# Optimization experiments

Hardware: AMD Instinct MI355X
Metric: run time of the kernel (lower is better)

Reference implementation:

```python
import jax, jax.numpy as jnp
import numpy as np

# Static multi-scale feature pyramid shapes (value_shapes arg of MSDeformAttn.forward)
VALUE_SHAPES = ((80, 80), (40, 40), (20, 20), (10, 10))
N_HEADS, N_LEVELS, N_POINTS, D_MODEL = 8, 4, 4, 256


def setup_inputs() -> dict:
    key = jax.random.key(0)
    ks = jax.random.split(key, 11)
    bs, lq, d = 16, 1000, D_MODEL
    lv = sum(h * w for h, w in VALUE_SHAPES)  # 8500
    s = 0.02  # weight scale
    f32 = jnp.float32
    return {
        "query": jax.random.normal(ks[0], (bs, lq, d), f32),
        "refer_bbox": jax.random.uniform(ks[1], (bs, lq, 1, 4), f32),  # cxcywh in [0,1]
        "value": jax.random.normal(ks[2], (bs, lv, d), f32),
        "W_off": jax.random.normal(ks[3], (d, N_HEADS * N_LEVELS * N_POINTS * 2), f32) * s,
        "b_off": jax.random.normal(ks[4], (N_HEADS * N_LEVELS * N_POINTS * 2,), f32) * s,
        "W_attn": jax.random.normal(ks[5], (d, N_HEADS * N_LEVELS * N_POINTS), f32) * s,
        "b_attn": jax.random.normal(ks[6], (N_HEADS * N_LEVELS * N_POINTS,), f32) * s,
        "W_val": jax.random.normal(ks[7], (d, d), f32) * s,
        "b_val": jax.random.normal(ks[8], (d,), f32) * s,
        "W_out": jax.random.normal(ks[9], (d, d), f32) * s,
        "b_out": jax.random.normal(ks[10], (d,), f32) * s,
    }


def _bilinear_sample(v, x, y):
    """grid_sample(mode=bilinear, padding=zeros, align_corners=False) equivalent.
    v: [bs, H, W, nh, dh]; x, y: pixel-space coords [bs, lq, nh, P].
    Returns [bs, lq, nh, P, dh]."""
    bs, H, W, nh, dh = v.shape
    x0f = jnp.floor(x)
    y0f = jnp.floor(y)
    wx = x - x0f  # fractional weights
    wy = y - y0f
    x0 = x0f.astype(jnp.int32)
    y0 = y0f.astype(jnp.int32)
    x1, y1 = x0 + 1, y0 + 1
    b_idx = jnp.arange(bs)[:, None, None, None]
    h_idx = jnp.arange(nh)[None, None, :, None]

    def gather(yi, xi):
        valid = (xi >= 0) & (xi < W) & (yi >= 0) & (yi < H)
        xc = jnp.clip(xi, 0, W - 1)
        yc = jnp.clip(yi, 0, H - 1)
        val = v[b_idx, yc, xc, h_idx]  # [bs, lq, nh, P, dh]
        return val * valid[..., None].astype(v.dtype)

    return (gather(y0, x0) * ((1 - wx) * (1 - wy))[..., None]
            + gather(y0, x1) * (wx * (1 - wy))[..., None]
            + gather(y1, x0) * ((1 - wx) * wy)[..., None]
            + gather(y1, x1) * (wx * wy)[..., None])


def reference(query, refer_bbox, value, W_off, b_off, W_attn, b_attn, W_val, b_val, W_out, b_out):
    bs, lq, d = query.shape
    nh, L, P = N_HEADS, N_LEVELS, N_POINTS
    dh = d // nh

    # value projection
    v = value @ W_val + b_val  # [bs, lv, d]
    v = v.reshape(bs, -1, nh, dh)

    # sampling offsets and attention weights from query
    offsets = (query @ W_off + b_off).reshape(bs, lq, nh, L, P, 2)
    attn = (query @ W_attn + b_attn).reshape(bs, lq, nh, L * P)
    attn = jax.nn.softmax(attn, axis=-1).reshape(bs, lq, nh, L, P)

    # refer_bbox: [bs, lq, 1, 4] cxcywh; num_points == 4 branch
    add = offsets / P * refer_bbox[:, :, None, :, None, 2:] * 0.5
    loc = refer_bbox[:, :, None, :, None, :2] + add  # [bs, lq, nh, L, P, 2] in [0,1]

    out = jnp.zeros((bs, lq, nh, dh), query.dtype)
    start = 0
    for l, (H, W) in enumerate(VALUE_SHAPES):
        vl = v[:, start:start + H * W].reshape(bs, H, W, nh, dh)
        start += H * W
        ll = loc[:, :, :, l]  # [bs, lq, nh, P, 2]
        # normalized [0,1] -> pixel coords (align_corners=False): p = loc*size - 0.5
        x = ll[..., 0] * W - 0.5
        y = ll[..., 1] * H - 0.5
        sampled = _bilinear_sample(vl, x, y)  # [bs, lq, nh, P, dh]
        out = out + jnp.einsum('bqhpd,bqhp->bqhd', sampled, attn[:, :, :, l])

    out = out.reshape(bs, lq, d)
    return out @ W_out + b_out
```

## Files before the change

### kernel.cpp

```cpp
#include <hip/hip_runtime.h>
#include <cstdint>
#include <cstddef>


typedef unsigned short u16;
typedef u16 u16x8 __attribute__((ext_vector_type(8)));
typedef __bf16 bf16x8 __attribute__((ext_vector_type(8)));
typedef float f32x4 __attribute__((ext_vector_type(4)));

__device__ inline u16 f2bf(float f) {
  return __builtin_bit_cast(u16, (__bf16)f);
}

__device__ __forceinline__ void glds16(const void* g, void* l) {
  __builtin_amdgcn_global_load_lds(
      (const __attribute__((address_space(1))) void*)g,
      (__attribute__((address_space(3))) void*)l, 16, 0, 0);
}

__global__ __launch_bounds__(256) void wconv(
    const float* __restrict__ W0, const float* __restrict__ W1,
    const float* __restrict__ W2, const float* __restrict__ W3,
    u16* __restrict__ T0, u16* __restrict__ T1, u16* __restrict__ T2,
    u16* __restrict__ T3) {
  __shared__ u16 tile[64][65];
  const float* Ws[4] = {W0, W1, W2, W3};
  u16* Ts[4] = {T0, T1, T2, T3};
  const int Ns[4] = {256, 256, 128, 256};
  const int z = blockIdx.z;
  const int N = Ns[z];
  const int n0 = blockIdx.x * 64;
  if (n0 >= N) return;
  const int k0 = blockIdx.y * 64;
  const float* W = Ws[z];
  u16* Wt = Ts[z];
  const int tr = threadIdx.x >> 6;
  const int tc = threadIdx.x & 63;
#pragma unroll
  for (int r = 0; r < 64; r += 4)
    tile[r + tr][tc] = f2bf(W[(size_t)(k0 + r + tr) * N + n0 + tc]);
  __syncthreads();
#pragma unroll
  for (int r = 0; r < 64; r += 4)
    Wt[(size_t)(n0 + r + tr) * 256 + k0 + tc] = tile[tc][r + tr];
}

template <int NF, bool OUT_BF16>
__global__ __launch_bounds__(256, 1) void gemm_pers(
    const float* __restrict__ A, const u16* __restrict__ Wt,
    const float* __restrict__ bias, void* __restrict__ Cv,
    int M, int NT, int G) {
  constexpr int N = NF * 16;
  __shared__ __align__(16) u16 Bls[N * 256];
  __shared__ __align__(16) float Asub[4 * 2 * 1024];
  const int wave = threadIdx.x >> 6;
  const int lane = threadIdx.x & 63;
  const int lr = lane & 15;
  const int lj = lane >> 4;

#pragma unroll
  for (int g = 0; g < NF * 2; ++g) {
    int inst = wave * NF * 2 + g;
    int s = inst * 2 + (lane >> 5);
    int pc = lane & 31;
    int jc = pc ^ (s & 7);
    int c = (s & 15) * NF + (s >> 4);
    glds16((const char*)Wt + (size_t)c * 512 + (size_t)jc * 16,
           (char*)Bls + inst * 1024);
  }

  float bv[NF];
#pragma unroll
  for (int ni = 0; ni < NF; ++ni) bv[ni] = bias[lr * NF + ni];

  char* aw = (char*)Asub + wave * 8192;

  auto stageA = [&](int t, int s, int buf) {
#pragma unroll
    for (int i = 0; i < 4; ++i) {
      long row = (long)t * 128 + wave * 32 + i * 8 + (lane >> 3);
      if (row > (long)M - 1) row = M - 1;
      int jc = (lane & 7) ^ (lane >> 3);
      glds16((const char*)A + row * 1024 + (size_t)s * 128 + (size_t)jc * 16,
             aw + buf * 4096 + i * 1024);
    }
  };

  stageA(blockIdx.x, 0, 0);
  stageA(blockIdx.x, 1, 1);
  __syncthreads();

  for (int t = blockIdx.x; t < NT; t += G) {
    f32x4 acc[2][NF] = {};
#pragma unroll
    for (int s = 0; s < 8; ++s) {
      if (s == 0 || s == 1)
        asm volatile("s_waitcnt vmcnt(20)" ::: "memory");
      else if (s == 2)
        asm volatile("s_waitcnt vmcnt(8)" ::: "memory");
      else
        asm volatile("s_waitcnt vmcnt(4)" ::: "memory");
      const char* ab = aw + (s & 1) * 4096;
      bf16x8 af[2];
#pragma unroll
      for (int rg = 0; rg < 2; ++rg) {
        int row = rg * 16 + lr;
        int sw = lane & 7;
        int j0 = lj * 2;
        f32x4 a0 = *(const f32x4*)(ab + row * 128 + ((j0 ^ sw) * 16));
        f32x4 a1 = *(const f32x4*)(ab + row * 128 + (((j0 + 1) ^ sw) * 16));
        bf16x8 v;
        v[0] = (__bf16)a0[0]; v[1] = (__bf16)a0[1];
        v[2] = (__bf16)a0[2]; v[3] = (__bf16)a0[3];
        v[4] = (__bf16)a1[0]; v[5] = (__bf16)a1[1];
        v[6] = (__bf16)a1[2]; v[7] = (__bf16)a1[3];
        af[rg] = v;
      }
#pragma unroll
      for (int ni = 0; ni < NF; ++ni) {
        int sl = ni * 16 + lr;
        int pc = (s * 4 + lj) ^ (sl & 7);
        bf16x8 b = __builtin_bit_cast(
            bf16x8, *(const u16x8*)((const char*)Bls + sl * 512 + pc * 16));
        acc[0][ni] = __builtin_amdgcn_mfma_f32_16x16x32_bf16(
            af[0], b, acc[0][ni], 0, 0, 0);
        acc[1][ni] = __builtin_amdgcn_mfma_f32_16x16x32_bf16(
            af[1], b, acc[1][ni], 0, 0, 0);
      }
      if (s < 6)
        stageA(t, s + 2, s & 1);
      else
        stageA(t + G, s - 6, s & 1);
    }
#pragma unroll
    for (int rg = 0; rg < 2; ++rg) {
#pragma unroll
      for (int r = 0; r < 4; ++r) {
        long grow = (long)t * 128 + wave * 32 + rg * 16 + lj * 4 + r;
        if (grow >= M) continue;
        if (OUT_BF16) {
          bf16x8 lo, hi;
#pragma unroll
          for (int j = 0; j < 8; ++j) {
            lo[j] = (__bf16)(acc[rg][j][r] + bv[j]);
            hi[j] = (__bf16)(acc[rg][8 + j][r] + bv[8 + j]);
          }
          u16* pC = (u16*)Cv + grow * N + lr * NF;
          *(u16x8*)pC = __builtin_bit_cast(u16x8, lo);
          *(u16x8*)(pC + 8) = __builtin_bit_cast(u16x8, hi);
        } else {
#pragma unroll
          for (int q = 0; q < NF / 4; ++q) {
            f32x4 v;
#pragma unroll
            for (int j = 0; j < 4; ++j)
              v[j] = acc[rg][q * 4 + j][r] + bv[q * 4 + j];
            *(f32x4*)((float*)Cv + grow * N + lr * NF + q * 4) = v;
          }
        }
      }
    }
  }
}

__global__ __launch_bounds__(256, 4) void sample_fused(
    const float* __restrict__ Lgo, const float* __restrict__ Lga,
    const float* __restrict__ bbox, const u16* __restrict__ vbf,
    float* __restrict__ outs) {
  const int t = threadIdx.x;
  const int bi = blockIdx.x;
  const int xcd = bi & 7;
  const int j = bi >> 3;
  const int half = (j >= 125) ? 1 : 0;
  const int batch = xcd + 8 * half;
  const int qb = j - 125 * half;
  const int i0 = (batch * 125 + qb) * 8;

  __shared__ __align__(16) float sa[8 * 128];
  __shared__ __align__(16) int4 soff[1024];
  __shared__ __align__(16) float4 sw4[1024];
  __shared__ float sb[32];
  if (t < 32) sb[t] = bbox[(size_t)i0 * 4 + t];
  ((float4*)sa)[t] = ((const float4*)(Lga + (size_t)i0 * 128))[t];
  __syncthreads();
  if (t < 64) {
    int base = (t >> 3) * 128 + (t & 7) * 16;
    float mx = -3.0e38f;
#pragma unroll
    for (int k = 0; k < 16; ++k) mx = fmaxf(mx, sa[base + k]);
    float e[16];
    float s = 0.f;
#pragma unroll
    for (int k = 0; k < 16; ++k) {
      e[k] = __expf(sa[base + k] - mx);
      s += e[k];
    }
    float inv = 1.f / s;
#pragma unroll
    for (int k = 0; k < 16; ++k) sa[base + k] = e[k] * inv;
  }
  __syncthreads();
#pragma unroll
  for (int it = 0; it < 4; ++it) {
    int idx = it * 256 + t;
    int ql = idx >> 7;
    int rest = idx & 127;
    int h = rest >> 4;
    int pt = rest & 15;
    int l = pt >> 2;
    int W = 80 >> l;
    float offx = Lgo[(size_t)(i0 + ql) * 256 + h * 32 + pt * 2];
    float offy = Lgo[(size_t)(i0 + ql) * 256 + h * 32 + pt * 2 + 1];
    float xf = (sb[ql * 4 + 0] + offx * 0.125f * sb[ql * 4 + 2]) * (float)W - 0.5f;
    float yf = (sb[ql * 4 + 1] + offy * 0.125f * sb[ql * 4 + 3]) * (float)W - 0.5f;
    float aw = sa[ql * 128 + h * 16 + pt];
    float x0f = floorf(xf), y0f = floorf(yf);
    float wx = xf - x0f, wy = yf - y0f;
    int x0 = (int)x0f, y0 = (int)y0f;
    int x1 = x0 + 1, y1 = y0 + 1;
    float fx0 = (x0 >= 0 && x0 < W) ? 1.f : 0.f;
    float fx1 = (x1 >= 0 && x1 < W) ? 1.f : 0.f;
    float fy0 = (y0 >= 0 && y0 < W) ? 1.f : 0.f;
    float fy1 = (y1 >= 0 && y1 < W) ? 1.f : 0.f;
    int xc0 = min(max(x0, 0), W - 1), xc1 = min(max(x1, 0), W - 1);
    int yc0 = min(max(y0, 0), W - 1), yc1 = min(max(y1, 0), W - 1);
    int baseb = ((25600 - (25600 >> (2 * l))) / 3) * 512;
    int4 o;
    o.x = baseb + (yc0 * W + xc0) * 512;
    o.y = baseb + (yc0 * W + xc1) * 512;
    o.z = baseb + (yc1 * W + xc0) * 512;
    o.w = baseb + (yc1 * W + xc1) * 512;
    float aw0 = aw * (1.f - wy), aw1 = aw * wy;
    float4 wv;
    wv.x = aw0 * (1.f - wx) * fx0 * fy0;
    wv.y = aw0 * wx * fx1 * fy0;
    wv.z = aw1 * (1.f - wx) * fx0 * fy1;
    wv.w = aw1 * wx * fx1 * fy1;
    int phys = ql * 128 + h * 16 + (pt ^ h);
    soff[phys] = o;
    sw4[phys] = wv;
  }
  __syncthreads();
  const int ql = t >> 5;
  const int r = t & 31;
  const int h = r >> 2;
  const int cg = r & 3;
  const int chb = (h * 32 + cg * 8) * 2;
  const char* vbb = (const char*)vbf + (size_t)batch * 8500 * 512 + chb;
  float acc[8] = {};
#pragma unroll 2
  for (int pt = 0; pt < 16; ++pt) {
    int phys = ql * 128 + h * 16 + (pt ^ h);
    int4 o = soff[phys];
    float4 wv = sw4[phys];
    uint4 v00 = *(const uint4*)(vbb + o.x);
    uint4 v01 = *(const uint4*)(vbb + o.y);
    uint4 v10 = *(const uint4*)(vbb + o.z);
    uint4 v11 = *(const uint4*)(vbb + o.w);
    const uint32_t* p00 = (const uint32_t*)&v00;
    const uint32_t* p01 = (const uint32_t*)&v01;
    const uint32_t* p10 = (const uint32_t*)&v10;
    const uint32_t* p11 = (const uint32_t*)&v11;
#pragma unroll
    for (int k = 0; k < 4; ++k) {
      float a0 = __uint_as_float(p00[k] << 16);
      float a1 = __uint_as_float(p00[k] & 0xffff0000u);
      float b0 = __uint_as_float(p01[k] << 16);
      float b1 = __uint_as_float(p01[k] & 0xffff0000u);
      float c0 = __uint_as_float(p10[k] << 16);
      float c1 = __uint_as_float(p10[k] & 0xffff0000u);
      float d0 = __uint_as_float(p11[k] << 16);
      float d1 = __uint_as_float(p11[k] & 0xffff0000u);
      acc[2 * k] += wv.x * a0 + wv.y * b0 + wv.z * c0 + wv.w * d0;
      acc[2 * k + 1] += wv.x * a1 + wv.y * b1 + wv.z * c1 + wv.w * d1;
    }
  }
  float4* op = (float4*)(outs + (size_t)(i0 + ql) * 256 + h * 32 + cg * 8);
  op[0] = make_float4(acc[0], acc[1], acc[2], acc[3]);
  op[1] = make_float4(acc[4], acc[5], acc[6], acc[7]);
}

extern "C" void kernel_launch(void* const* d_in, const int* in_sizes, int n_in,
                              void* d_out, int out_size, void* d_ws, size_t ws_size,
                              hipStream_t stream) {
  const float* query  = (const float*)d_in[0];
  const float* bbox   = (const float*)d_in[1];
  const float* value  = (const float*)d_in[2];
  const float* W_off  = (const float*)d_in[3];
  const float* b_off  = (const float*)d_in[4];
  const float* W_attn = (const float*)d_in[5];
  const float* b_attn = (const float*)d_in[6];
  const float* W_val  = (const float*)d_in[7];
  const float* b_val  = (const float*)d_in[8];
  const float* W_out  = (const float*)d_in[9];
  const float* b_out  = (const float*)d_in[10];
  float* out = (float*)d_out;

  char* w = (char*)d_ws;
  u16* vbf     = (u16*)w;
  float* Lgo   = (float*)(w + 69632000);
  float* Lga   = (float*)(w + 86016000);
  float* outs  = (float*)(w + 94208000);
  u16* Wt_val  = (u16*)(w + 110592000);
  u16* Wt_off  = (u16*)(w + 110723072);
  u16* Wt_attn = (u16*)(w + 110854144);
  u16* Wt_out  = (u16*)(w + 110919680);

  const int M_v = 16 * 8500;
  const int M_q = 16 * 1000;

  wconv<<<dim3(4, 4, 4), 256, 0, stream>>>(W_val, W_off, W_attn, W_out,
                                           Wt_val, Wt_off, Wt_attn, Wt_out);
  gemm_pers<16, true><<<256, 256, 0, stream>>>(
      value, Wt_val, b_val, (void*)vbf, M_v, 1063, 256);
  gemm_pers<16, false><<<125, 256, 0, stream>>>(
      query, Wt_off, b_off, (void*)Lgo, M_q, 125, 125);
  gemm_pers<8, false><<<125, 256, 0, stream>>>(
      query, Wt_attn, b_attn, (void*)Lga, M_q, 125, 125);
  sample_fused<<<2000, 256, 0, stream>>>(Lgo, Lga, bbox, vbf, outs);
  gemm_pers<16, false><<<125, 256, 0, stream>>>(
      outs, Wt_out, b_out, (void*)out, M_q, 125, 125);
}
```

Measured before the change: 133.3 us.

## Retile persistent GEMMs to 16 rows per wave with configurable wave count

The persistent bf16 MFMA GEMM is generalized into a template over wave count, with each wave now computing 16 rows instead of 32. The value projection uses 8 waves per block (128-row tiles) and the query-side GEMMs use 4 waves with 64-row tiles across 250 blocks. The aim is more parallel blocks for the small M=16000 GEMMs and lower register pressure per wave. In exchange, each B-fragment load from LDS feeds only one MFMA rather than two, and the vmcnt wait counts had to be retuned by hand for the new number of loads in flight.

```diff
diff --git a/kernel.cpp b/kernel.cpp
--- a/kernel.cpp
+++ b/kernel.cpp
@@ -45,26 +45,29 @@
     Wt[(size_t)(n0 + r + tr) * 256 + k0 + tc] = tile[tc][r + tr];
 }
 
-template <int NF, bool OUT_BF16>
-__global__ __launch_bounds__(256, 1) void gemm_pers(
+template <int WAVES, int NF, bool OUT_BF16>
+__global__ __launch_bounds__(WAVES * 64, 1) void gemm_p2(
     const float* __restrict__ A, const u16* __restrict__ Wt,
     const float* __restrict__ bias, void* __restrict__ Cv,
     int M, int NT, int G) {
   constexpr int N = NF * 16;
+  constexpr int TR = WAVES * 16;
+  constexpr int STN = OUT_BF16 ? (NF / 2) : NF;
   __shared__ __align__(16) u16 Bls[N * 256];
-  __shared__ __align__(16) float Asub[4 * 2 * 1024];
+  __shared__ __align__(16) float Asub[WAVES * 1024];
   const int wave = threadIdx.x >> 6;
   const int lane = threadIdx.x & 63;
   const int lr = lane & 15;
   const int lj = lane >> 4;
 
-#pragma unroll
-  for (int g = 0; g < NF * 2; ++g) {
-    int inst = wave * NF * 2 + g;
-    int s = inst * 2 + (lane >> 5);
+  constexpr int NI = NF * 8 / WAVES;
+#pragma unroll
+  for (int g = 0; g < NI; ++g) {
+    int inst = wave * NI + g;
+    int s2 = inst * 2 + (lane >> 5);
     int pc = lane & 31;
-    int jc = pc ^ (s & 7);
-    int c = (s & 15) * NF + (s >> 4);
+    int jc = pc ^ (s2 & 7);
+    int c = (s2 & 15) * NF + (s2 >> 4);
     glds16((const char*)Wt + (size_t)c * 512 + (size_t)jc * 16,
            (char*)Bls + inst * 1024);
   }
@@ -73,16 +76,16 @@
 #pragma unroll
   for (int ni = 0; ni < NF; ++ni) bv[ni] = bias[lr * NF + ni];
 
-  char* aw = (char*)Asub + wave * 8192;
+  char* aw = (char*)Asub + wave * 4096;
 
   auto stageA = [&](int t, int s, int buf) {
 #pragma unroll
-    for (int i = 0; i < 4; ++i) {
-      long row = (long)t * 128 + wave * 32 + i * 8 + (lane >> 3);
+    for (int i = 0; i < 2; ++i) {
+      long row = (long)t * TR + wave * 16 + i * 8 + (lane >> 3);
       if (row > (long)M - 1) row = M - 1;
       int jc = (lane & 7) ^ (lane >> 3);
       glds16((const char*)A + row * 1024 + (size_t)s * 128 + (size_t)jc * 16,
-             aw + buf * 4096 + i * 1024);
+             aw + buf * 2048 + i * 1024);
     }
   };
 
@@ -91,72 +94,64 @@
   __syncthreads();
 
   for (int t = blockIdx.x; t < NT; t += G) {
-    f32x4 acc[2][NF] = {};
+    f32x4 acc[NF] = {};
 #pragma unroll
     for (int s = 0; s < 8; ++s) {
-      if (s == 0 || s == 1)
-        asm volatile("s_waitcnt vmcnt(20)" ::: "memory");
-      else if (s == 2)
-        asm volatile("s_waitcnt vmcnt(8)" ::: "memory");
-      else
-        asm volatile("s_waitcnt vmcnt(4)" ::: "memory");
-      const char* ab = aw + (s & 1) * 4096;
-      bf16x8 af[2];
-#pragma unroll
-      for (int rg = 0; rg < 2; ++rg) {
-        int row = rg * 16 + lr;
-        int sw = lane & 7;
-        int j0 = lj * 2;
-        f32x4 a0 = *(const f32x4*)(ab + row * 128 + ((j0 ^ sw) * 16));
-        f32x4 a1 = *(const f32x4*)(ab + row * 128 + (((j0 + 1) ^ sw) * 16));
-        bf16x8 v;
-        v[0] = (__bf16)a0[0]; v[1] = (__bf16)a0[1];
-        v[2] = (__bf16)a0[2]; v[3] = (__bf16)a0[3];
-        v[4] = (__bf16)a1[0]; v[5] = (__bf16)a1[1];
-        v[6] = (__bf16)a1[2]; v[7] = (__bf16)a1[3];
-        af[rg] = v;
+      if (s < 2) {
+        if constexpr (STN == 8)
+          asm volatile("s_waitcnt vmcnt(10)" ::: "memory");
+        else
+          asm volatile("s_waitcnt vmcnt(18)" ::: "memory");
+      } else {
+        asm volatile("s_waitcnt vmcnt(2)" ::: "memory");
       }
+      const char* ab = aw + (s & 1) * 2048;
+      const int sw = lr & 7;
+      const int j0 = lj * 2;
+      f32x4 a0 = *(const f32x4*)(ab + lr * 128 + ((j0 ^ sw) * 16));
+      f32x4 a1 = *(const f32x4*)(ab + lr * 128 + (((j0 + 1) ^ sw) * 16));
+      bf16x8 af;
+      af[0] = (__bf16)a0[0]; af[1] = (__bf16)a0[1];
+      af[2] = (__bf16)a0[2]; af[3] = (__bf16)a0[3];
+      af[4] = (__bf16)a1[0]; af[5] = (__bf16)a1[1];
+      af[6] = (__bf16)a1[2]; af[7] = (__bf16)a1[3];
 #pragma unroll
       for (int ni = 0; ni < NF; ++ni) {
         int sl = ni * 16 + lr;
         int pc = (s * 4 + lj) ^ (sl & 7);
         bf16x8 b = __builtin_bit_cast(
             bf16x8, *(const u16x8*)((const char*)Bls + sl * 512 + pc * 16));
-        acc[0][ni] = __builtin_amdgcn_mfma_f32_16x16x32_bf16(
-            af[0], b, acc[0][ni], 0, 0, 0);
-        acc[1][ni] = __builtin_amdgcn_mfma_f32_16x16x32_bf16(
-            af[1], b, acc[1][ni], 0, 0, 0);
+        acc[ni] = __builtin_amdgcn_mfma_f32_16x16x32_bf16(af, b, acc[ni],
+                                                          0, 0, 0);
       }
       if (s < 6)
         stageA(t, s + 2, s & 1);
+      else if (s == 6)
+        stageA(t + G, 0, 0);
       else
-        stageA(t + G, s - 6, s & 1);
-    }
-#pragma unroll
-    for (int rg = 0; rg < 2; ++rg) {
-#pragma unroll
-      for (int r = 0; r < 4; ++r) {
-        long grow = (long)t * 128 + wave * 32 + rg * 16 + lj * 4 + r;
-        if (grow >= M) continue;
-        if (OUT_BF16) {
-          bf16x8 lo, hi;
-#pragma unroll
-          for (int j = 0; j < 8; ++j) {
-            lo[j] = (__bf16)(acc[rg][j][r] + bv[j]);
-            hi[j] = (__bf16)(acc[rg][8 + j][r] + bv[8 + j]);
-          }
-          u16* pC = (u16*)Cv + grow * N + lr * NF;
-          *(u16x8*)pC = __builtin_bit_cast(u16x8, lo);
-          *(u16x8*)(pC + 8) = __builtin_bit_cast(u16x8, hi);
-        } else {
-#pragma unroll
-          for (int q = 0; q < NF / 4; ++q) {
-            f32x4 v;
-#pragma unroll
-            for (int j = 0; j < 4; ++j)
-              v[j] = acc[rg][q * 4 + j][r] + bv[q * 4 + j];
-            *(f32x4*)((float*)Cv + grow * N + lr * NF + q * 4) = v;
-          }
+        stageA(t + G, 1, 1);
+    }
+#pragma unroll
+    for (int r = 0; r < 4; ++r) {
+      long grow = (long)t * TR + wave * 16 + lj * 4 + r;
+      if (grow >= M) continue;
+      if (OUT_BF16) {
+        bf16x8 lo, hi;
+#pragma unroll
+        for (int j = 0; j < 8; ++j) {
+          lo[j] = (__bf16)(acc[j][r] + bv[j]);
+          hi[j] = (__bf16)(acc[8 + j][r] + bv[8 + j]);
+        }
+        u16* pC = (u16*)Cv + grow * N + lr * NF;
+        *(u16x8*)pC = __builtin_bit_cast(u16x8, lo);
+        *(u16x8*)(pC + 8) = __builtin_bit_cast(u16x8, hi);
+      } else {
+#pragma unroll
+        for (int q = 0; q < NF / 4; ++q) {
+          f32x4 v;
+#pragma unroll
+          for (int j = 0; j < 4; ++j) v[j] = acc[q * 4 + j][r] + bv[q * 4 + j];
+          *(f32x4*)((float*)Cv + grow * N + lr * NF + q * 4) = v;
         }
       }
     }
@@ -311,13 +306,13 @@
 
   wconv<<<dim3(4, 4, 4), 256, 0, stream>>>(W_val, W_off, W_attn, W_out,
                                            Wt_val, Wt_off, Wt_attn, Wt_out);
-  gemm_pers<16, true><<<256, 256, 0, stream>>>(
+  gemm_p2<8, 16, true><<<256, 512, 0, stream>>>(
       value, Wt_val, b_val, (void*)vbf, M_v, 1063, 256);
-  gemm_pers<16, false><<<125, 256, 0, stream>>>(
-      query, Wt_off, b_off, (void*)Lgo, M_q, 125, 125);
-  gemm_pers<8, false><<<125, 256, 0, stream>>>(
-      query, Wt_attn, b_attn, (void*)Lga, M_q, 125, 125);
+  gemm_p2<4, 16, false><<<250, 256, 0, stream>>>(
+      query, Wt_off, b_off, (void*)Lgo, M_q, 250, 250);
+  gemm_p2<4, 8, false><<<250, 256, 0, stream>>>(
+      query, Wt_attn, b_attn, (void*)Lga, M_q, 250, 250);
   sample_fused<<<2000, 256, 0, stream>>>(Lgo, Lga, bbox, vbf, outs);
-  gemm_pers<16, false><<<125, 256, 0, stream>>>(
-      outs, Wt_out, b_out, (void*)out, M_q, 125, 125);
-}
+  gemm_p2<4, 16, false><<<250, 256, 0, stream>>>(
+      outs, Wt_out, b_out, (void*)out, M_q, 250, 250);
+}
```

Result: faster. 124.7 us (-6.4%).
